# Performance work log

Measured on AMD Instinct MI355X. Metric: run time of the kernel, lower is better.

## Reference

```python
import jax, jax.numpy as jnp
import numpy as np

SEQ, D, H, DFF, L, MAXINT = 8, 2, 2, 32, 2, 255
V = MAXINT + 1
BATCH = 131072


def _layer_norm(x, g, b, eps=1e-5):
    mu = jnp.mean(x, axis=-1, keepdims=True)
    var = jnp.mean((x - mu) ** 2, axis=-1, keepdims=True)
    return (x - mu) / jnp.sqrt(var + eps) * g + b


def setup_inputs() -> dict:
    key = jax.random.key(0)
    ks = jax.random.split(key, 8)
    f = lambda k, shape: (jax.random.normal(k, shape, dtype=jnp.float32) * 0.2)
    x = jax.random.randint(ks[0], (BATCH, SEQ), 0, 256)
    return {
        "x": x,
        "Wqkv": f(ks[1], (L, 3 * D, D)), "bqkv": jnp.zeros((L, 3 * D), jnp.float32),
        "Wo": f(ks[2], (L, D, D)), "bo": jnp.zeros((L, D), jnp.float32),
        "W1": f(ks[3], (L, DFF, D)), "b1": jnp.zeros((L, DFF), jnp.float32),
        "W2": f(ks[4], (L, D, DFF)), "b2": jnp.zeros((L, D), jnp.float32),
        "g1": jnp.ones((L, D), jnp.float32), "be1": jnp.zeros((L, D), jnp.float32),
        "g2": jnp.ones((L, D), jnp.float32), "be2": jnp.zeros((L, D), jnp.float32),
        "Wout": f(ks[5], (V, D)), "bout": jnp.zeros((V,), jnp.float32),
    }


def reference(x, Wqkv, bqkv, Wo, bo, W1, b1, W2, b2, g1, be1, g2, be2, Wout, bout):
    B, S = x.shape
    hd = D // H                      # head_dim = 1
    scale = 1.0 / np.sqrt(hd)
    numbers = x.astype(jnp.float32) / MAXINT
    positions = jnp.broadcast_to(jnp.arange(S, dtype=jnp.float32) / (S - 1), (B, S))
    h = jnp.stack([numbers, positions], axis=-1)  # [B, S, D]

    for l in range(L):  # small fixed layer count
        qkv = h @ Wqkv[l].T + bqkv[l]             # [B, S, 3D]
        q, k, v = jnp.split(qkv, 3, axis=-1)
        sh = lambda t: t.reshape(B, S, H, hd).transpose(0, 2, 1, 3)  # [B,H,S,hd]
        q, k, v = sh(q), sh(k), sh(v)
        scores = jnp.einsum('bhqd,bhkd->bhqk', q, k) * scale
        attn = jax.nn.softmax(scores, axis=-1)
        o = jnp.einsum('bhqk,bhkd->bhqd', attn, v)
        o = o.transpose(0, 2, 1, 3).reshape(B, S, D) @ Wo[l].T + bo[l]
        h = _layer_norm(h + o, g1[l], be1[l])      # post-norm (norm_first=False)
        ff = jax.nn.gelu(h @ W1[l].T + b1[l], approximate=False) @ W2[l].T + b2[l]
        h = _layer_norm(h + ff, g2[l], be2[l])

    final = h[:, -1]                               # [B, D]
    return final @ Wout.T + bout                   # [B, V]
```

## Files before the change

### kernel.cpp

```cpp
#include <hip/hip_runtime.h>
#include <math.h>

#define SEQ   8
#define DFF   32
#define NL    2
#define VOCAB 256
#define BATCH 131072

__device__ __forceinline__ float gelu_f(float t) {
    float ax = fabsf(t);
    float k  = __builtin_amdgcn_rcpf(fmaf(0.3275911f, ax, 1.0f));
    float p  = fmaf(k, 1.061405429f, -1.453152027f);
    p = fmaf(k, p, 1.421413741f);
    p = fmaf(k, p, -0.284496736f);
    p = fmaf(k, p, 0.254829592f);
    p = p * k;
    float e  = __builtin_amdgcn_exp2f(-1.44269504f * ax * ax);
    float er = copysignf(fmaf(-p, e, 1.0f), t);
    return 0.5f * t * (1.0f + er);
}

__global__ __launch_bounds__(256, 8) void seqtx_one(
    const int*   __restrict__ x,
    const float* __restrict__ Wqkv, const float* __restrict__ bqkv,
    const float* __restrict__ Wo,   const float* __restrict__ bo,
    const float* __restrict__ W1,   const float* __restrict__ b1,
    const float* __restrict__ W2,   const float* __restrict__ b2,
    const float* __restrict__ g1,   const float* __restrict__ be1,
    const float* __restrict__ g2,   const float* __restrict__ be2,
    const float* __restrict__ Wout, const float* __restrict__ bout,
    float* __restrict__ out)
{
    __shared__ float4 exch[256];

    const int tid   = threadIdx.x;
    const int sub   = tid & 7;
    const int gid   = blockIdx.x * 256 + tid;
    const int lane  = tid & 63;
    const int g8    = (tid >> 3) & 7;
    const int gbase = tid & ~7;

    const int cg = lane * 4;
    const float2* wvp = reinterpret_cast<const float2*>(Wout);
    float2 wv0 = wvp[cg + 0];
    float2 wv1 = wvp[cg + 1];
    float2 wv2 = wvp[cg + 2];
    float2 wv3 = wvp[cg + 3];
    float4 bv  = *reinterpret_cast<const float4*>(bout + cg);

    float h0 = (float)x[gid] * (1.0f / 255.0f);
    float h1 = (float)sub * (1.0f / 7.0f);

    float ndl;

    {
        const float* wq = Wqkv;
        const float* bq = bqkv;
        float q0 = fmaf(wq[0],  h0, fmaf(wq[1],  h1, bq[0]));
        float q1 = fmaf(wq[2],  h0, fmaf(wq[3],  h1, bq[1]));
        float k0 = fmaf(wq[4],  h0, fmaf(wq[5],  h1, bq[2]));
        float k1 = fmaf(wq[6],  h0, fmaf(wq[7],  h1, bq[3]));
        float v0 = fmaf(wq[8],  h0, fmaf(wq[9],  h1, bq[4]));
        float v1 = fmaf(wq[10], h0, fmaf(wq[11], h1, bq[5]));

        exch[gbase | ((sub + g8) & 7)] = make_float4(k0, v0, k1, v1);
        __builtin_amdgcn_wave_barrier();

        float q0e = q0 * 1.44269504f;
        float q1e = q1 * 1.44269504f;
        float s0 = 0.0f, a0 = 0.0f, s1 = 0.0f, a1 = 0.0f;
        #pragma unroll
        for (int j = 0; j < SEQ; ++j) {
            float4 kv = exch[gbase | ((j + g8) & 7)];
            float e0 = __builtin_amdgcn_exp2f(q0e * kv.x);
            s0 += e0;  a0 = fmaf(e0, kv.y, a0);
            float e1 = __builtin_amdgcn_exp2f(q1e * kv.z);
            s1 += e1;  a1 = fmaf(e1, kv.w, a1);
        }
        float o0 = a0 * __builtin_amdgcn_rcpf(s0);
        float o1 = a1 * __builtin_amdgcn_rcpf(s1);

        float p0 = fmaf(Wo[0], o0, fmaf(Wo[1], o1, bo[0]));
        float p1 = fmaf(Wo[2], o0, fmaf(Wo[3], o1, bo[1]));
        float a = h0 + p0, c = h1 + p1;
        float d = 0.5f * (a - c);
        float nd = d * __builtin_amdgcn_rsqf(fmaf(d, d, 1e-5f));
        h0 = fmaf( nd, g1[0], be1[0]);
        h1 = fmaf(-nd, g1[1], be1[1]);

        float f0 = b2[0], f1 = b2[1];
        for (int j = 0; j < DFF; ++j) {
            float t = fmaf(W1[j * 2], h0, fmaf(W1[j * 2 + 1], h1, b1[j]));
            float g = gelu_f(t);
            f0 = fmaf(g, W2[j], f0);
            f1 = fmaf(g, W2[32 + j], f1);
        }

        a = h0 + f0;  c = h1 + f1;
        d = 0.5f * (a - c);
        float nd2 = d * __builtin_amdgcn_rsqf(fmaf(d, d, 1e-5f));
        h0 = fmaf( nd2, g2[0], be2[0]);
        h1 = fmaf(-nd2, g2[1], be2[1]);
    }

    {
        const float* wq = Wqkv + 12;
        const float* bq = bqkv + 6;
        float q0 = fmaf(wq[0],  h0, fmaf(wq[1],  h1, bq[0]));
        float q1 = fmaf(wq[2],  h0, fmaf(wq[3],  h1, bq[1]));
        float k0 = fmaf(wq[4],  h0, fmaf(wq[5],  h1, bq[2]));
        float k1 = fmaf(wq[6],  h0, fmaf(wq[7],  h1, bq[3]));
        float v0 = fmaf(wq[8],  h0, fmaf(wq[9],  h1, bq[4]));
        float v1 = fmaf(wq[10], h0, fmaf(wq[11], h1, bq[5]));

        float q0e = __shfl(q0, 7, SEQ) * 1.44269504f;
        float q1e = __shfl(q1, 7, SEQ) * 1.44269504f;
        float e0 = __builtin_amdgcn_exp2f(q0e * k0);
        float e1 = __builtin_amdgcn_exp2f(q1e * k1);
        float n0 = e0 * v0, n1 = e1 * v1;
        #pragma unroll
        for (int m = 1; m < SEQ; m <<= 1) {
            e0 += __shfl_xor(e0, m, SEQ);
            n0 += __shfl_xor(n0, m, SEQ);
            e1 += __shfl_xor(e1, m, SEQ);
            n1 += __shfl_xor(n1, m, SEQ);
        }
        float o0 = n0 * __builtin_amdgcn_rcpf(e0);
        float o1 = n1 * __builtin_amdgcn_rcpf(e1);

        float hp0 = __shfl(h0, 7, SEQ);
        float hp1 = __shfl(h1, 7, SEQ);
        float p0 = fmaf(Wo[4], o0, fmaf(Wo[5], o1, bo[2]));
        float p1 = fmaf(Wo[6], o0, fmaf(Wo[7], o1, bo[3]));
        float a = hp0 + p0, c = hp1 + p1;
        float d = 0.5f * (a - c);
        float nd = d * __builtin_amdgcn_rsqf(fmaf(d, d, 1e-5f));
        float hh0 = fmaf( nd, g1[2], be1[2]);
        float hh1 = fmaf(-nd, g1[3], be1[3]);

        float f0p = 0.0f, f1p = 0.0f;
        #pragma unroll
        for (int m = 0; m < 4; ++m) {
            int j = sub + m * 8;
            float t = fmaf(W1[64 + j * 2], hh0, fmaf(W1[64 + j * 2 + 1], hh1, b1[32 + j]));
            float g = gelu_f(t);
            f0p = fmaf(g, W2[64 + j], f0p);
            f1p = fmaf(g, W2[96 + j], f1p);
        }
        #pragma unroll
        for (int m = 1; m < SEQ; m <<= 1) {
            f0p += __shfl_xor(f0p, m, SEQ);
            f1p += __shfl_xor(f1p, m, SEQ);
        }
        float f0 = f0p + b2[2];
        float f1 = f1p + b2[3];

        a = hh0 + f0;  c = hh1 + f1;
        d = 0.5f * (a - c);
        ndl = d * __builtin_amdgcn_rsqf(fmaf(d, d, 1e-5f));
    }

    float gf0 = g2[2], gf1 = g2[3], bf0 = be2[2], bf1 = be2[3];
    float u0 = wv0.x * gf0 - wv0.y * gf1,  w0 = fmaf(wv0.x, bf0, fmaf(wv0.y, bf1, bv.x));
    float u1 = wv1.x * gf0 - wv1.y * gf1,  w1 = fmaf(wv1.x, bf0, fmaf(wv1.y, bf1, bv.y));
    float u2 = wv2.x * gf0 - wv2.y * gf1,  w2 = fmaf(wv2.x, bf0, fmaf(wv2.y, bf1, bv.z));
    float u3 = wv3.x * gf0 - wv3.y * gf1,  w3 = fmaf(wv3.x, bf0, fmaf(wv3.y, bf1, bv.w));

    const size_t rowbase = (size_t)(gid >> 6) * 8;
    #pragma unroll
    for (int e = 0; e < 8; ++e) {
        float ndv = __int_as_float(
            __builtin_amdgcn_readlane(__float_as_int(ndl), e * 8 + 7));
        float4 res;
        res.x = fmaf(ndv, u0, w0);
        res.y = fmaf(ndv, u1, w1);
        res.z = fmaf(ndv, u2, w2);
        res.w = fmaf(ndv, u3, w3);
        *reinterpret_cast<float4*>(&out[(rowbase + e) * VOCAB + cg]) = res;
    }
}

extern "C" void kernel_launch(void* const* d_in, const int* in_sizes, int n_in,
                              void* d_out, int out_size, void* d_ws, size_t ws_size,
                              hipStream_t stream) {
    const int*   x    = (const int*)  d_in[0];
    const float* Wqkv = (const float*)d_in[1];
    const float* bqkv = (const float*)d_in[2];
    const float* Wo   = (const float*)d_in[3];
    const float* bo   = (const float*)d_in[4];
    const float* W1   = (const float*)d_in[5];
    const float* b1   = (const float*)d_in[6];
    const float* W2   = (const float*)d_in[7];
    const float* b2   = (const float*)d_in[8];
    const float* g1   = (const float*)d_in[9];
    const float* be1  = (const float*)d_in[10];
    const float* g2   = (const float*)d_in[11];
    const float* be2  = (const float*)d_in[12];
    const float* Wout = (const float*)d_in[13];
    const float* bout = (const float*)d_in[14];
    float* out = (float*)d_out;

    seqtx_one<<<BATCH / 32, 256, 0, stream>>>(
        x, Wqkv, bqkv, Wo, bo, W1, b1, W2, b2, g1, be1, g2, be2, Wout, bout, out);
}
```

Measured before the change: 34.04 us.

## Process four 8-sample chunks per wave in a loop to amortize setup

```diff
diff --git a/kernel.cpp b/kernel.cpp
--- a/kernel.cpp
+++ b/kernel.cpp
@@ -1,11 +1,11 @@
 #include <hip/hip_runtime.h>
 #include <math.h>
 
-#define SEQ   8
-#define DFF   32
-#define NL    2
-#define VOCAB 256
-#define BATCH 131072
+#define SEQ    8
+#define DFF    32
+#define VOCAB  256
+#define BATCH  131072
+#define CHUNKS 4
 
 __device__ __forceinline__ float gelu_f(float t) {
     float ax = fabsf(t);
@@ -20,7 +20,7 @@
     return 0.5f * t * (1.0f + er);
 }
 
-__global__ __launch_bounds__(256, 8) void seqtx_one(
+__global__ __launch_bounds__(256, 8) void seqtx_pipe(
     const int*   __restrict__ x,
     const float* __restrict__ Wqkv, const float* __restrict__ bqkv,
     const float* __restrict__ Wo,   const float* __restrict__ bo,
@@ -34,149 +34,153 @@
     __shared__ float4 exch[256];
 
     const int tid   = threadIdx.x;
+    const int lane  = tid & 63;
+    const int wid   = tid >> 6;
     const int sub   = tid & 7;
-    const int gid   = blockIdx.x * 256 + tid;
-    const int lane  = tid & 63;
     const int g8    = (tid >> 3) & 7;
     const int gbase = tid & ~7;
-
-    const int cg = lane * 4;
+    const int cg    = lane * 4;
+
     const float2* wvp = reinterpret_cast<const float2*>(Wout);
     float2 wv0 = wvp[cg + 0];
     float2 wv1 = wvp[cg + 1];
     float2 wv2 = wvp[cg + 2];
     float2 wv3 = wvp[cg + 3];
     float4 bv  = *reinterpret_cast<const float4*>(bout + cg);
-
-    float h0 = (float)x[gid] * (1.0f / 255.0f);
-    float h1 = (float)sub * (1.0f / 7.0f);
-
-    float ndl;
-
-    {
-        const float* wq = Wqkv;
-        const float* bq = bqkv;
-        float q0 = fmaf(wq[0],  h0, fmaf(wq[1],  h1, bq[0]));
-        float q1 = fmaf(wq[2],  h0, fmaf(wq[3],  h1, bq[1]));
-        float k0 = fmaf(wq[4],  h0, fmaf(wq[5],  h1, bq[2]));
-        float k1 = fmaf(wq[6],  h0, fmaf(wq[7],  h1, bq[3]));
-        float v0 = fmaf(wq[8],  h0, fmaf(wq[9],  h1, bq[4]));
-        float v1 = fmaf(wq[10], h0, fmaf(wq[11], h1, bq[5]));
-
-        exch[gbase | ((sub + g8) & 7)] = make_float4(k0, v0, k1, v1);
-        __builtin_amdgcn_wave_barrier();
-
-        float q0e = q0 * 1.44269504f;
-        float q1e = q1 * 1.44269504f;
-        float s0 = 0.0f, a0 = 0.0f, s1 = 0.0f, a1 = 0.0f;
-        #pragma unroll
-        for (int j = 0; j < SEQ; ++j) {
-            float4 kv = exch[gbase | ((j + g8) & 7)];
-            float e0 = __builtin_amdgcn_exp2f(q0e * kv.x);
-            s0 += e0;  a0 = fmaf(e0, kv.y, a0);
-            float e1 = __builtin_amdgcn_exp2f(q1e * kv.z);
-            s1 += e1;  a1 = fmaf(e1, kv.w, a1);
-        }
-        float o0 = a0 * __builtin_amdgcn_rcpf(s0);
-        float o1 = a1 * __builtin_amdgcn_rcpf(s1);
-
-        float p0 = fmaf(Wo[0], o0, fmaf(Wo[1], o1, bo[0]));
-        float p1 = fmaf(Wo[2], o0, fmaf(Wo[3], o1, bo[1]));
-        float a = h0 + p0, c = h1 + p1;
-        float d = 0.5f * (a - c);
-        float nd = d * __builtin_amdgcn_rsqf(fmaf(d, d, 1e-5f));
-        h0 = fmaf( nd, g1[0], be1[0]);
-        h1 = fmaf(-nd, g1[1], be1[1]);
-
-        float f0 = b2[0], f1 = b2[1];
-        for (int j = 0; j < DFF; ++j) {
-            float t = fmaf(W1[j * 2], h0, fmaf(W1[j * 2 + 1], h1, b1[j]));
-            float g = gelu_f(t);
-            f0 = fmaf(g, W2[j], f0);
-            f1 = fmaf(g, W2[32 + j], f1);
-        }
-
-        a = h0 + f0;  c = h1 + f1;
-        d = 0.5f * (a - c);
-        float nd2 = d * __builtin_amdgcn_rsqf(fmaf(d, d, 1e-5f));
-        h0 = fmaf( nd2, g2[0], be2[0]);
-        h1 = fmaf(-nd2, g2[1], be2[1]);
-    }
-
-    {
-        const float* wq = Wqkv + 12;
-        const float* bq = bqkv + 6;
-        float q0 = fmaf(wq[0],  h0, fmaf(wq[1],  h1, bq[0]));
-        float q1 = fmaf(wq[2],  h0, fmaf(wq[3],  h1, bq[1]));
-        float k0 = fmaf(wq[4],  h0, fmaf(wq[5],  h1, bq[2]));
-        float k1 = fmaf(wq[6],  h0, fmaf(wq[7],  h1, bq[3]));
-        float v0 = fmaf(wq[8],  h0, fmaf(wq[9],  h1, bq[4]));
-        float v1 = fmaf(wq[10], h0, fmaf(wq[11], h1, bq[5]));
-
-        float q0e = __shfl(q0, 7, SEQ) * 1.44269504f;
-        float q1e = __shfl(q1, 7, SEQ) * 1.44269504f;
-        float e0 = __builtin_amdgcn_exp2f(q0e * k0);
-        float e1 = __builtin_amdgcn_exp2f(q1e * k1);
-        float n0 = e0 * v0, n1 = e1 * v1;
-        #pragma unroll
-        for (int m = 1; m < SEQ; m <<= 1) {
-            e0 += __shfl_xor(e0, m, SEQ);
-            n0 += __shfl_xor(n0, m, SEQ);
-            e1 += __shfl_xor(e1, m, SEQ);
-            n1 += __shfl_xor(n1, m, SEQ);
-        }
-        float o0 = n0 * __builtin_amdgcn_rcpf(e0);
-        float o1 = n1 * __builtin_amdgcn_rcpf(e1);
-
-        float hp0 = __shfl(h0, 7, SEQ);
-        float hp1 = __shfl(h1, 7, SEQ);
-        float p0 = fmaf(Wo[4], o0, fmaf(Wo[5], o1, bo[2]));
-        float p1 = fmaf(Wo[6], o0, fmaf(Wo[7], o1, bo[3]));
-        float a = hp0 + p0, c = hp1 + p1;
-        float d = 0.5f * (a - c);
-        float nd = d * __builtin_amdgcn_rsqf(fmaf(d, d, 1e-5f));
-        float hh0 = fmaf( nd, g1[2], be1[2]);
-        float hh1 = fmaf(-nd, g1[3], be1[3]);
-
-        float f0p = 0.0f, f1p = 0.0f;
-        #pragma unroll
-        for (int m = 0; m < 4; ++m) {
-            int j = sub + m * 8;
-            float t = fmaf(W1[64 + j * 2], hh0, fmaf(W1[64 + j * 2 + 1], hh1, b1[32 + j]));
-            float g = gelu_f(t);
-            f0p = fmaf(g, W2[64 + j], f0p);
-            f1p = fmaf(g, W2[96 + j], f1p);
-        }
-        #pragma unroll
-        for (int m = 1; m < SEQ; m <<= 1) {
-            f0p += __shfl_xor(f0p, m, SEQ);
-            f1p += __shfl_xor(f1p, m, SEQ);
-        }
-        float f0 = f0p + b2[2];
-        float f1 = f1p + b2[3];
-
-        a = hh0 + f0;  c = hh1 + f1;
-        d = 0.5f * (a - c);
-        ndl = d * __builtin_amdgcn_rsqf(fmaf(d, d, 1e-5f));
-    }
-
     float gf0 = g2[2], gf1 = g2[3], bf0 = be2[2], bf1 = be2[3];
     float u0 = wv0.x * gf0 - wv0.y * gf1,  w0 = fmaf(wv0.x, bf0, fmaf(wv0.y, bf1, bv.x));
     float u1 = wv1.x * gf0 - wv1.y * gf1,  w1 = fmaf(wv1.x, bf0, fmaf(wv1.y, bf1, bv.y));
     float u2 = wv2.x * gf0 - wv2.y * gf1,  w2 = fmaf(wv2.x, bf0, fmaf(wv2.y, bf1, bv.z));
     float u3 = wv3.x * gf0 - wv3.y * gf1,  w3 = fmaf(wv3.x, bf0, fmaf(wv3.y, bf1, bv.w));
 
-    const size_t rowbase = (size_t)(gid >> 6) * 8;
-    #pragma unroll
-    for (int e = 0; e < 8; ++e) {
-        float ndv = __int_as_float(
-            __builtin_amdgcn_readlane(__float_as_int(ndl), e * 8 + 7));
-        float4 res;
-        res.x = fmaf(ndv, u0, w0);
-        res.y = fmaf(ndv, u1, w1);
-        res.z = fmaf(ndv, u2, w2);
-        res.w = fmaf(ndv, u3, w3);
-        *reinterpret_cast<float4*>(&out[(rowbase + e) * VOCAB + cg]) = res;
+    int ebase = (blockIdx.x * 4 + wid) * 32;
+
+    for (int c = 0; c < CHUNKS; ++c, ebase += 8) {
+        float h0 = (float)x[ebase * SEQ + lane] * (1.0f / 255.0f);
+        float h1 = (float)sub * (1.0f / 7.0f);
+        float ndl;
+
+        {
+            const float* wq = Wqkv;
+            const float* bq = bqkv;
+            float q0 = fmaf(wq[0],  h0, fmaf(wq[1],  h1, bq[0]));
+            float q1 = fmaf(wq[2],  h0, fmaf(wq[3],  h1, bq[1]));
+            float k0 = fmaf(wq[4],  h0, fmaf(wq[5],  h1, bq[2]));
+            float k1 = fmaf(wq[6],  h0, fmaf(wq[7],  h1, bq[3]));
+            float v0 = fmaf(wq[8],  h0, fmaf(wq[9],  h1, bq[4]));
+            float v1 = fmaf(wq[10], h0, fmaf(wq[11], h1, bq[5]));
+
+            __builtin_amdgcn_wave_barrier();
+            exch[gbase | ((sub + g8) & 7)] = make_float4(k0, v0, k1, v1);
+            __builtin_amdgcn_wave_barrier();
+
+            float q0e = q0 * 1.44269504f;
+            float q1e = q1 * 1.44269504f;
+            float s0 = 0.0f, a0 = 0.0f, s1 = 0.0f, a1 = 0.0f;
+            #pragma unroll
+            for (int j = 0; j < SEQ; ++j) {
+                float4 kv = exch[gbase | ((j + g8) & 7)];
+                float e0 = __builtin_amdgcn_exp2f(q0e * kv.x);
+                s0 += e0;  a0 = fmaf(e0, kv.y, a0);
+                float e1 = __builtin_amdgcn_exp2f(q1e * kv.z);
+                s1 += e1;  a1 = fmaf(e1, kv.w, a1);
+            }
+            float o0 = a0 * __builtin_amdgcn_rcpf(s0);
+            float o1 = a1 * __builtin_amdgcn_rcpf(s1);
+
+            float p0 = fmaf(Wo[0], o0, fmaf(Wo[1], o1, bo[0]));
+            float p1 = fmaf(Wo[2], o0, fmaf(Wo[3], o1, bo[1]));
+            float a = h0 + p0, cc = h1 + p1;
+            float d = 0.5f * (a - cc);
+            float nd = d * __builtin_amdgcn_rsqf(fmaf(d, d, 1e-5f));
+            h0 = fmaf( nd, g1[0], be1[0]);
+            h1 = fmaf(-nd, g1[1], be1[1]);
+
+            float f0 = b2[0], f1 = b2[1];
+            for (int j = 0; j < DFF; ++j) {
+                float t = fmaf(W1[j * 2], h0, fmaf(W1[j * 2 + 1], h1, b1[j]));
+                float g = gelu_f(t);
+                f0 = fmaf(g, W2[j], f0);
+                f1 = fmaf(g, W2[32 + j], f1);
+            }
+
+            a = h0 + f0;  cc = h1 + f1;
+            d = 0.5f * (a - cc);
+            float nd2 = d * __builtin_amdgcn_rsqf(fmaf(d, d, 1e-5f));
+            h0 = fmaf( nd2, g2[0], be2[0]);
+            h1 = fmaf(-nd2, g2[1], be2[1]);
+        }
+
+        {
+            const float* wq = Wqkv + 12;
+            const float* bq = bqkv + 6;
+            float q0 = fmaf(wq[0],  h0, fmaf(wq[1],  h1, bq[0]));
+            float q1 = fmaf(wq[2],  h0, fmaf(wq[3],  h1, bq[1]));
+            float k0 = fmaf(wq[4],  h0, fmaf(wq[5],  h1, bq[2]));
+            float k1 = fmaf(wq[6],  h0, fmaf(wq[7],  h1, bq[3]));
+            float v0 = fmaf(wq[8],  h0, fmaf(wq[9],  h1, bq[4]));
+            float v1 = fmaf(wq[10], h0, fmaf(wq[11], h1, bq[5]));
+
+            float q0e = __shfl(q0, 7, SEQ) * 1.44269504f;
+            float q1e = __shfl(q1, 7, SEQ) * 1.44269504f;
+            float e0 = __builtin_amdgcn_exp2f(q0e * k0);
+            float e1 = __builtin_amdgcn_exp2f(q1e * k1);
+            float n0 = e0 * v0, n1 = e1 * v1;
+            #pragma unroll
+            for (int m = 1; m < SEQ; m <<= 1) {
+                e0 += __shfl_xor(e0, m, SEQ);
+                n0 += __shfl_xor(n0, m, SEQ);
+                e1 += __shfl_xor(e1, m, SEQ);
+                n1 += __shfl_xor(n1, m, SEQ);
+            }
+            float o0 = n0 * __builtin_amdgcn_rcpf(e0);
+            float o1 = n1 * __builtin_amdgcn_rcpf(e1);
+
+            float hp0 = __shfl(h0, 7, SEQ);
+            float hp1 = __shfl(h1, 7, SEQ);
+            float p0 = fmaf(Wo[4], o0, fmaf(Wo[5], o1, bo[2]));
+            float p1 = fmaf(Wo[6], o0, fmaf(Wo[7], o1, bo[3]));
+            float a = hp0 + p0, cc = hp1 + p1;
+            float d = 0.5f * (a - cc);
+            float nd = d * __builtin_amdgcn_rsqf(fmaf(d, d, 1e-5f));
+            float hh0 = fmaf( nd, g1[2], be1[2]);
+            float hh1 = fmaf(-nd, g1[3], be1[3]);
+
+            float f0p = 0.0f, f1p = 0.0f;
+            #pragma unroll
+            for (int m = 0; m < 4; ++m) {
+                int j = sub + m * 8;
+                float t = fmaf(W1[64 + j * 2], hh0, fmaf(W1[64 + j * 2 + 1], hh1, b1[32 + j]));
+                float g = gelu_f(t);
+                f0p = fmaf(g, W2[64 + j], f0p);
+                f1p = fmaf(g, W2[96 + j], f1p);
+            }
+            #pragma unroll
+            for (int m = 1; m < SEQ; m <<= 1) {
+                f0p += __shfl_xor(f0p, m, SEQ);
+                f1p += __shfl_xor(f1p, m, SEQ);
+            }
+            float f0 = f0p + b2[2];
+            float f1 = f1p + b2[3];
+
+            a = hh0 + f0;  cc = hh1 + f1;
+            d = 0.5f * (a - cc);
+            ndl = d * __builtin_amdgcn_rsqf(fmaf(d, d, 1e-5f));
+        }
+
+        float* dst = out + (size_t)ebase * VOCAB + cg;
+        #pragma unroll
+        for (int e = 0; e < SEQ; ++e) {
+            float ndv = __int_as_float(
+                __builtin_amdgcn_readlane(__float_as_int(ndl), e * 8 + 7));
+            float4 res;
+            res.x = fmaf(ndv, u0, w0);
+            res.y = fmaf(ndv, u1, w1);
+            res.z = fmaf(ndv, u2, w2);
+            res.w = fmaf(ndv, u3, w3);
+            *reinterpret_cast<float4*>(dst) = res;
+            dst += VOCAB;
+        }
     }
 }
 
@@ -200,6 +204,6 @@
     const float* bout = (const float*)d_in[14];
     float* out = (float*)d_out;
 
-    seqtx_one<<<BATCH / 32, 256, 0, stream>>>(
+    seqtx_pipe<<<BATCH / (32 * CHUNKS), 256, 0, stream>>>(
         x, Wqkv, bqkv, Wo, bo, W1, b1, W2, b2, g1, be1, g2, be2, Wout, bout, out);
 }
```

After: 40.14 us. 17.9% more time.
